# Performance work log

Hardware: AMD Instinct MI355X
Metric: run time of the kernel (lower is better)

## Reference

```python
import jax, jax.numpy as jnp
import numpy as np

N, E, R = 50000, 800000, 3
D, H = 128, 128
NUM_SHAPE, NUM_COLOR, MAX_POS = 16, 8, 25
B, NUM_CLASS = 256, 10
EPS = 1e-5


def setup_inputs() -> dict:
    key = jax.random.key(0)
    ks = jax.random.split(key, 24)
    s = lambda fan: 1.0 / np.sqrt(fan)
    inp = {
        "x_idx": jax.random.randint(ks[0], (N, 3), 0, 8),
        "edge_index": jax.random.randint(ks[1], (2, E), 0, N),
        "edge_type": jax.random.randint(ks[2], (E,), 0, R),
        "batch": jnp.sort(jax.random.randint(ks[3], (N,), 0, B)),
        "shape_emb": jax.random.normal(ks[4], (NUM_SHAPE, D), jnp.float32),
        "color_emb": jax.random.normal(ks[5], (NUM_COLOR, D), jnp.float32),
        "pos_emb": jax.random.normal(ks[6], (MAX_POS, D), jnp.float32),
        "W1": jax.random.normal(ks[7], (R, D, H), jnp.float32) * s(D),
        "root1": jax.random.normal(ks[8], (D, H), jnp.float32) * s(D),
        "b1": jax.random.normal(ks[9], (H,), jnp.float32) * 0.01,
        "g1": jax.random.uniform(ks[10], (H,), jnp.float32, 0.5, 1.5),
        "beta1": jax.random.normal(ks[11], (H,), jnp.float32) * 0.1,
        "m1": jax.random.normal(ks[12], (H,), jnp.float32) * 0.1,
        "v1": jax.random.uniform(ks[13], (H,), jnp.float32, 0.5, 1.5),
        "W2": jax.random.normal(ks[14], (R, H, H), jnp.float32) * s(H),
        "root2": jax.random.normal(ks[15], (H, H), jnp.float32) * s(H),
        "b2": jax.random.normal(ks[16], (H,), jnp.float32) * 0.01,
        "g2": jax.random.uniform(ks[17], (H,), jnp.float32, 0.5, 1.5),
        "beta2": jax.random.normal(ks[18], (H,), jnp.float32) * 0.1,
        "m2": jax.random.normal(ks[19], (H,), jnp.float32) * 0.1,
        "v2": jax.random.uniform(ks[20], (H,), jnp.float32, 0.5, 1.5),
        "clsW": jax.random.normal(ks[21], (H, NUM_CLASS), jnp.float32) * s(H),
        "clsb": jax.random.normal(ks[22], (NUM_CLASS,), jnp.float32) * 0.01,
    }
    return inp


def rgcn_conv(x, edge_index, edge_type, W, root, b):
    # per-relation transform, gather at src, mean-scatter at dst (PyG RGCNConv, aggr='mean')
    src, dst = edge_index[0], edge_index[1]
    xw = jnp.einsum('nd,rdh->rnh', x, W)            # [R, N, H]
    msg = xw[edge_type, src]                        # [E, H]
    seg = dst * R + edge_type                       # segment per (dst, relation)
    ssum = jax.ops.segment_sum(msg, seg, num_segments=N * R)
    cnt = jax.ops.segment_sum(jnp.ones((E,), x.dtype), seg, num_segments=N * R)
    mean = jnp.where(cnt[:, None] > 0, ssum / jnp.maximum(cnt, 1.0)[:, None], 0.0)
    agg = mean.reshape(N, R, -1).sum(axis=1)        # sum over relations of per-relation means
    return agg + x @ root + b


def batchnorm_eval(x, g, beta, m, v):
    return g * (x - m) * jax.lax.rsqrt(v + EPS) + beta


def reference(x_idx, edge_index, edge_type, batch, shape_emb, color_emb, pos_emb,
              W1, root1, b1, g1, beta1, m1, v1,
              W2, root2, b2, g2, beta2, m2, v2, clsW, clsb):
    x = (shape_emb[x_idx[:, 0]] + color_emb[x_idx[:, 1]]
         + pos_emb[jnp.clip(x_idx[:, 2], 0, MAX_POS - 1)])
    x = jax.nn.relu(batchnorm_eval(rgcn_conv(x, edge_index, edge_type, W1, root1, b1),
                                   g1, beta1, m1, v1))
    x = jax.nn.relu(batchnorm_eval(rgcn_conv(x, edge_index, edge_type, W2, root2, b2),
                                   g2, beta2, m2, v2))
    hsum = jax.ops.segment_sum(x, batch, num_segments=B)
    hcnt = jax.ops.segment_sum(jnp.ones((N,), x.dtype), batch, num_segments=B)
    hg = hsum / jnp.maximum(hcnt, 1.0)[:, None]     # global mean pool [B, H]
    return hg @ clsW + clsb
```

## Files before the change

kernel.cpp:

```cpp
#include <hip/hip_runtime.h>

#define N_NODES 50000
#define E_EDGES 800000
#define R_REL 3
#define NSEG (N_NODES * R_REL)
#define DH 128
#define KDIM 512
#define ROWB 1024
#define XOFF (3 * DH * 2)
#define BATCHES 256
#define NCLASS 10
#define EPSV 1e-5f

#define BSHIFT 9
#define BNODES 512
#define NBUCK ((N_NODES + BNODES - 1) / BNODES)
#define SEGB (BNODES * R_REL)
#define CAP 9216
#define NCHUNK 128
#define CHUNK (E_EDGES / NCHUNK)
#define MATN (NBUCK * NCHUNK)

typedef __attribute__((ext_vector_type(8))) short short8v;
typedef __attribute__((ext_vector_type(4))) unsigned uint4v;
typedef __attribute__((ext_vector_type(4))) float float4v;
typedef unsigned short ushort_t;

__device__ __forceinline__ ushort_t f2bf(float f) {
    union { float f; unsigned u; } x; x.f = f;
    unsigned r = x.u + 0x7FFFu + ((x.u >> 16) & 1u);
    return (ushort_t)(r >> 16);
}
__device__ __forceinline__ float bf2f(ushort_t h) {
    union { unsigned u; float f; } x; x.u = ((unsigned)h) << 16;
    return x.f;
}
__device__ __forceinline__ float u2f(unsigned u) {
    union { unsigned u; float f; } x; x.u = u;
    return x.f;
}

__global__ void build_x_kernel(const int* __restrict__ xi,
                               const float* __restrict__ se,
                               const float* __restrict__ ce,
                               const float* __restrict__ pe,
                               ushort_t* __restrict__ A) {
    int tid = blockIdx.x * blockDim.x + threadIdx.x;
    int node = tid >> 4, c = tid & 15;
    if (node >= N_NODES) return;
    int i0 = xi[node * 3 + 0];
    int i1 = xi[node * 3 + 1];
    int i2 = xi[node * 3 + 2];
    i2 = i2 < 0 ? 0 : (i2 > 24 ? 24 : i2);
    const float4* sa = reinterpret_cast<const float4*>(se + (size_t)i0 * DH + c * 8);
    const float4* sb = reinterpret_cast<const float4*>(ce + (size_t)i1 * DH + c * 8);
    const float4* sp = reinterpret_cast<const float4*>(pe + (size_t)i2 * DH + c * 8);
    short8v o;
    #pragma unroll
    for (int q = 0; q < 2; ++q) {
        float4 a = sa[q], b = sb[q], p = sp[q];
        o[q * 4 + 0] = (short)f2bf(a.x + b.x + p.x);
        o[q * 4 + 1] = (short)f2bf(a.y + b.y + p.y);
        o[q * 4 + 2] = (short)f2bf(a.z + b.z + p.z);
        o[q * 4 + 3] = (short)f2bf(a.w + b.w + p.w);
    }
    *reinterpret_cast<short8v*>(A + (size_t)node * KDIM + 3 * DH + c * 8) = o;
}

__global__ __launch_bounds__(512) void chunk_hist_kernel(const int* __restrict__ ei,
                                                         int* __restrict__ mat) {
    __shared__ int lh[NBUCK];
    int t = threadIdx.x, blk = blockIdx.x;
    if (t < NBUCK) lh[t] = 0;
    __syncthreads();
    int base = blk * CHUNK;
    for (int i = t; i < CHUNK; i += 512)
        atomicAdd(&lh[ei[E_EDGES + base + i] >> BSHIFT], 1);
    __syncthreads();
    if (t < NBUCK) mat[t * NCHUNK + blk] = lh[t];
}

__global__ __launch_bounds__(1024) void matscan_kernel(int* __restrict__ mat,
                                                       int* __restrict__ bbase,
                                                       int* __restrict__ offs3) {
    __shared__ int partial[1024];
    int t = threadIdx.x;
    int buf[13];
    int base = t * 13;
    int s = 0;
    #pragma unroll
    for (int j = 0; j < 13; ++j) {
        int idx = base + j;
        int v = (idx < MATN) ? mat[idx] : 0;
        buf[j] = s;
        s += v;
    }
    partial[t] = s;
    __syncthreads();
    for (int d = 1; d < 1024; d <<= 1) {
        int u = (t >= d) ? partial[t - d] : 0;
        __syncthreads();
        partial[t] += u;
        __syncthreads();
    }
    int off = (t > 0) ? partial[t - 1] : 0;
    #pragma unroll
    for (int j = 0; j < 13; ++j) {
        int idx = base + j;
        if (idx < MATN) mat[idx] = off + buf[j];
    }
    __syncthreads();
    if (t < NBUCK) bbase[t] = mat[t * NCHUNK];
    if (t == 0) { bbase[NBUCK] = E_EDGES; offs3[NSEG] = E_EDGES; }
}

__global__ __launch_bounds__(512) void chunk_scatter_kernel(const int* __restrict__ ei,
                                                            const int* __restrict__ et,
                                                            const int* __restrict__ mat,
                                                            int* __restrict__ tlist) {
    __shared__ int sorted[CHUNK];
    __shared__ int lh[NBUCK];
    __shared__ int lstart[NBUCK + 1];
    __shared__ int mbase[NBUCK];
    __shared__ int scr[128];
    int t = threadIdx.x, blk = blockIdx.x;
    if (t < NBUCK) { lh[t] = 0; mbase[t] = mat[t * NCHUNK + blk]; }
    __syncthreads();
    int base = blk * CHUNK;
    for (int i = t; i < CHUNK; i += 512)
        atomicAdd(&lh[ei[E_EDGES + base + i] >> BSHIFT], 1);
    __syncthreads();
    if (t < 128) scr[t] = (t < NBUCK) ? lh[t] : 0;
    __syncthreads();
    for (int d = 1; d < 128; d <<= 1) {
        int u = 0;
        if (t < 128 && t >= d) u = scr[t - d];
        __syncthreads();
        if (t < 128) scr[t] += u;
        __syncthreads();
    }
    if (t < NBUCK) lstart[t] = scr[t] - lh[t];
    if (t == NBUCK - 1) lstart[NBUCK] = scr[t];
    __syncthreads();
    if (t < NBUCK) lh[t] = lstart[t];
    __syncthreads();
    for (int i = t; i < CHUNK; i += 512) {
        int e = base + i;
        int src = ei[e];
        int dst = ei[E_EDGES + e];
        int r = et[e];
        int b = dst >> BSHIFT;
        int ls = (dst & (BNODES - 1)) * R_REL + r;
        int p = atomicAdd(&lh[b], 1);
        sorted[p] = (ls << 16) | src;
    }
    __syncthreads();
    for (int i = t; i < CHUNK; i += 512) {
        int lo = 0, hi = NBUCK - 1;
        while (lo < hi) {
            int mid = (lo + hi + 1) >> 1;
            if (lstart[mid] <= i) lo = mid; else hi = mid - 1;
        }
        tlist[mbase[lo] + (i - lstart[lo])] = sorted[i];
    }
}

__global__ __launch_bounds__(512) void localsort_kernel(const int* __restrict__ tlist,
                                                        const int* __restrict__ bbase,
                                                        int* __restrict__ offs3,
                                                        int* __restrict__ elist) {
    __shared__ int hist[SEGB];
    __shared__ int scr[512];
    __shared__ int tl[CAP];
    __shared__ int el[CAP];
    int b = blockIdx.x, t = threadIdx.x;
    int ebeg = bbase[b], eend = bbase[b + 1];
    int cnt = eend - ebeg;
    int segbase = b * SEGB;
    #pragma unroll
    for (int j = 0; j < 3; ++j) hist[t + j * 512] = 0;
    __syncthreads();

    bool fit = (cnt <= CAP);
    if (fit) {
        for (int i = t; i < cnt; i += 512) {
            int pk = tlist[ebeg + i];
            tl[i] = pk;
            atomicAdd(&hist[pk >> 16], 1);
        }
    } else {
        for (int i = t; i < cnt; i += 512)
            atomicAdd(&hist[tlist[ebeg + i] >> 16], 1);
    }
    __syncthreads();
    int h0 = hist[3 * t], h1 = hist[3 * t + 1], h2 = hist[3 * t + 2];
    int s = h0 + h1 + h2;
    scr[t] = s;
    __syncthreads();
    for (int d = 1; d < 512; d <<= 1) {
        int u = (t >= d) ? scr[t - d] : 0;
        __syncthreads();
        scr[t] += u;
        __syncthreads();
    }
    int off = (t > 0) ? scr[t - 1] : 0;
    int e0 = off, e1 = off + h0, e2 = off + h0 + h1;
    {
        int sg = segbase + 3 * t;
        if (sg < NSEG)     offs3[sg]     = ebeg + e0;
        if (sg + 1 < NSEG) offs3[sg + 1] = ebeg + e1;
        if (sg + 2 < NSEG) offs3[sg + 2] = ebeg + e2;
    }
    __syncthreads();
    hist[3 * t] = e0; hist[3 * t + 1] = e1; hist[3 * t + 2] = e2;
    __syncthreads();
    if (fit) {
        for (int i = t; i < cnt; i += 512) {
            int pk = tl[i];
            int pos = atomicAdd(&hist[pk >> 16], 1);
            el[pos] = (pk & 0xFFFF) * ROWB + XOFF;
        }
        __syncthreads();
        for (int i = t; i < cnt; i += 512)
            elist[ebeg + i] = el[i];
    } else {
        for (int i = t; i < cnt; i += 512) {
            int pk = tlist[ebeg + i];
            int pos = atomicAdd(&hist[pk >> 16], 1);
            elist[ebeg + pos] = (pk & 0xFFFF) * ROWB + XOFF;
        }
    }
}

__global__ void setup_kernel(const float* __restrict__ W1, const float* __restrict__ root1,
                             const float* __restrict__ W2, const float* __restrict__ root2,
                             ushort_t* __restrict__ Wf1, ushort_t* __restrict__ Wf2,
                             const int* __restrict__ batch, int* __restrict__ bstart,
                             const float* __restrict__ b1, const float* __restrict__ g1,
                             const float* __restrict__ be1, const float* __restrict__ m1,
                             const float* __restrict__ v1,
                             const float* __restrict__ b2, const float* __restrict__ g2,
                             const float* __restrict__ be2, const float* __restrict__ m2,
                             const float* __restrict__ v2,
                             float* __restrict__ sc1, float* __restrict__ sh1,
                             float* __restrict__ sc2, float* __restrict__ sh2) {
    int tid = blockIdx.x * blockDim.x + threadIdx.x;
    if (tid < 16384) {
        int L = tid >> 13;
        int rem = tid & 8191;
        int l = rem & 63;
        int nt = (rem >> 6) & 7;
        int ks = rem >> 9;
        const float* W = L ? W2 : W1;
        const float* root = L ? root2 : root1;
        ushort_t* dst = (L ? Wf2 : Wf1) + (size_t)rem * 8;
        int col = nt * 16 + (l & 15);
        int kb = ks * 32 + (l >> 4) * 8;
        short8v o;
        #pragma unroll
        for (int j = 0; j < 8; ++j) {
            int k = kb + j;
            float w = (k < 384) ? W[(size_t)k * DH + col] : root[(size_t)(k - 384) * DH + col];
            o[j] = (short)f2bf(w);
        }
        *reinterpret_cast<short8v*>(dst) = o;
    } else if (tid < 16384 + BATCHES + 1) {
        int b = tid - 16384;
        int lo = 0, hi = N_NODES;
        while (lo < hi) {
            int mid = (lo + hi) >> 1;
            if (batch[mid] < b) lo = mid + 1; else hi = mid;
        }
        bstart[b] = lo;
    } else if (tid < 16384 + 257 + DH) {
        int c = tid - 16384 - 257;
        float s = g1[c] * rsqrtf(v1[c] + EPSV);
        sc1[c] = s;
        sh1[c] = (b1[c] - m1[c]) * s + be1[c];
    } else if (tid < 16384 + 257 + 2 * DH) {
        int c = tid - 16384 - 257 - DH;
        float s = g2[c] * rsqrtf(v2[c] + EPSV);
        sc2[c] = s;
        sh2[c] = (b2[c] - m2[c]) * s + be2[c];
    }
}

__global__ __launch_bounds__(256) void agg_kernel(const char* __restrict__ Ab,
                                                  const int* __restrict__ offs3,
                                                  const int* __restrict__ elist,
                                                  char* __restrict__ Aob) {
    int t = threadIdx.x;
    int g = t >> 4, c = t & 15;
    int n = blockIdx.x * 16 + g;
    if (n >= N_NODES) return;
    int s0 = offs3[3 * n + 0];
    int s1 = offs3[3 * n + 1];
    int s2 = offs3[3 * n + 2];
    int s3 = offs3[3 * n + 3];
    int cb = c * 16;

    float S0 = 0, S1 = 0, S2 = 0, S3 = 0, S4 = 0, S5 = 0, S6 = 0, S7 = 0;
    float p0 = 0, p1 = 0, p2 = 0, p3 = 0, p4 = 0, p5 = 0, p6 = 0, p7 = 0;
    float q0 = 0, q1 = 0, q2 = 0, q3 = 0, q4 = 0, q5 = 0, q6 = 0, q7 = 0;

    #define ACC8(V)                                           \
        S0 += u2f(V[0] << 16); S1 += u2f(V[0] & 0xFFFF0000u); \
        S2 += u2f(V[1] << 16); S3 += u2f(V[1] & 0xFFFF0000u); \
        S4 += u2f(V[2] << 16); S5 += u2f(V[2] & 0xFFFF0000u); \
        S6 += u2f(V[3] << 16); S7 += u2f(V[3] & 0xFFFF0000u);
    #define SNAPCHK(E)                                                              \
        if ((E) == s1) { p0=S0; p1=S1; p2=S2; p3=S3; p4=S4; p5=S5; p6=S6; p7=S7; }  \
        if ((E) == s2) { q0=S0; q1=S1; q2=S2; q3=S3; q4=S4; q5=S5; q6=S6; q7=S7; }

    int i = s0;
    int bend = s0 + ((s3 - s0) & ~3);
    if (i < bend) {
        int j0 = elist[i], j1 = elist[i + 1], j2 = elist[i + 2], j3 = elist[i + 3];
        uint4v g0 = *reinterpret_cast<const uint4v*>(Ab + j0 + cb);
        uint4v g1 = *reinterpret_cast<const uint4v*>(Ab + j1 + cb);
        uint4v g2 = *reinterpret_cast<const uint4v*>(Ab + j2 + cb);
        uint4v g3 = *reinterpret_cast<const uint4v*>(Ab + j3 + cb);
        for (;;) {
            int inx = i + 4;
            bool more = inx < bend;
            uint4v h0, h1, h2, h3;
            if (more) {
                int k0 = elist[inx], k1 = elist[inx + 1], k2 = elist[inx + 2], k3 = elist[inx + 3];
                h0 = *reinterpret_cast<const uint4v*>(Ab + k0 + cb);
                h1 = *reinterpret_cast<const uint4v*>(Ab + k1 + cb);
                h2 = *reinterpret_cast<const uint4v*>(Ab + k2 + cb);
                h3 = *reinterpret_cast<const uint4v*>(Ab + k3 + cb);
            }
            SNAPCHK(i)     ACC8(g0)
            SNAPCHK(i + 1) ACC8(g1)
            SNAPCHK(i + 2) ACC8(g2)
            SNAPCHK(i + 3) ACC8(g3)
            if (!more) break;
            g0 = h0; g1 = h1; g2 = h2; g3 = h3;
            i = inx;
        }
        i = bend;
    }
    for (; i < s3; ++i) {
        int j = elist[i];
        uint4v v = *reinterpret_cast<const uint4v*>(Ab + j + cb);
        SNAPCHK(i)
        ACC8(v)
    }
    if (s1 == s3) { p0=S0; p1=S1; p2=S2; p3=S3; p4=S4; p5=S5; p6=S6; p7=S7; }
    if (s2 == s3) { q0=S0; q1=S1; q2=S2; q3=S3; q4=S4; q5=S5; q6=S6; q7=S7; }
    #undef ACC8
    #undef SNAPCHK

    int c0 = s1 - s0, c1 = s2 - s1, c2 = s3 - s2;
    float i0 = c0 ? 1.f / c0 : 0.f;
    float i1 = c1 ? 1.f / c1 : 0.f;
    float i2 = c2 ? 1.f / c2 : 0.f;
    char* base = Aob + (size_t)n * ROWB + cb;
    uint4v o;
    o[0] = (unsigned)f2bf(p0 * i0) | ((unsigned)f2bf(p1 * i0) << 16);
    o[1] = (unsigned)f2bf(p2 * i0) | ((unsigned)f2bf(p3 * i0) << 16);
    o[2] = (unsigned)f2bf(p4 * i0) | ((unsigned)f2bf(p5 * i0) << 16);
    o[3] = (unsigned)f2bf(p6 * i0) | ((unsigned)f2bf(p7 * i0) << 16);
    *reinterpret_cast<uint4v*>(base + 0 * 256) = o;
    o[0] = (unsigned)f2bf((q0 - p0) * i1) | ((unsigned)f2bf((q1 - p1) * i1) << 16);
    o[1] = (unsigned)f2bf((q2 - p2) * i1) | ((unsigned)f2bf((q3 - p3) * i1) << 16);
    o[2] = (unsigned)f2bf((q4 - p4) * i1) | ((unsigned)f2bf((q5 - p5) * i1) << 16);
    o[3] = (unsigned)f2bf((q6 - p6) * i1) | ((unsigned)f2bf((q7 - p7) * i1) << 16);
    *reinterpret_cast<uint4v*>(base + 1 * 256) = o;
    o[0] = (unsigned)f2bf((S0 - q0) * i2) | ((unsigned)f2bf((S1 - q1) * i2) << 16);
    o[1] = (unsigned)f2bf((S2 - q2) * i2) | ((unsigned)f2bf((S3 - q3) * i2) << 16);
    o[2] = (unsigned)f2bf((S4 - q4) * i2) | ((unsigned)f2bf((S5 - q5) * i2) << 16);
    o[3] = (unsigned)f2bf((S6 - q6) * i2) | ((unsigned)f2bf((S7 - q7) * i2) << 16);
    *reinterpret_cast<uint4v*>(base + 2 * 256) = o;
}

__global__ __launch_bounds__(256) void gemm_mfma_kernel(const ushort_t* __restrict__ A,
                                                        const ushort_t* __restrict__ Wf,
                                                        const float* __restrict__ sc,
                                                        const float* __restrict__ sh,
                                                        ushort_t* __restrict__ Aout) {
    int w = threadIdx.x >> 6, l = threadIdx.x & 63;
    int base = blockIdx.x * 64 + w * 16;
    int arow = base + (l & 15);
    if (arow >= N_NODES) arow = N_NODES - 1;
    const short8v* ap = reinterpret_cast<const short8v*>(A + (size_t)arow * KDIM + (l >> 4) * 8);
    const short8v* wf = reinterpret_cast<const short8v*>(Wf) + l;

    float4v acc[8];
    #pragma unroll
    for (int nt = 0; nt < 8; ++nt) acc[nt] = (float4v){0.f, 0.f, 0.f, 0.f};

    #pragma unroll 4
    for (int ks = 0; ks < 16; ++ks) {
        short8v a = ap[ks * 4];
        const short8v* bp = wf + ks * 512;
        #pragma unroll
        for (int nt = 0; nt < 8; ++nt) {
            short8v b = bp[nt * 64];
            acc[nt] = __builtin_amdgcn_mfma_f32_16x16x32_bf16(a, b, acc[nt], 0, 0, 0);
        }
    }

    int colb = l & 15;
    int rowq = (l >> 4) * 4;
    #pragma unroll
    for (int nt = 0; nt < 8; ++nt) {
        int col = nt * 16 + colb;
        float scv = sc[col], shv = sh[col];
        #pragma unroll
        for (int r = 0; r < 4; ++r) {
            int row = base + rowq + r;
            if (row < N_NODES) {
                float val = fmaxf(acc[nt][r] * scv + shv, 0.f);
                Aout[(size_t)row * KDIM + 3 * DH + col] = f2bf(val);
            }
        }
    }
}

__global__ __launch_bounds__(256) void pool_cls_kernel(
        const ushort_t* __restrict__ h,
        const int* __restrict__ bstart,
        const float* __restrict__ clsW,
        const float* __restrict__ clsb,
        float* __restrict__ out) {
    __shared__ float hsh[DH];
    int b = blockIdx.x;
    int t = threadIdx.x;
    int c = t & 127;
    int half = t >> 7;
    int beg = bstart[b], end = bstart[b + 1];
    float s = 0.f;
    for (int n = beg + half; n < end; n += 2)
        s += bf2f(h[(size_t)n * KDIM + c]);
    if (half == 1) hsh[c] = s;
    __syncthreads();
    if (half == 0) {
        float cnt = (float)(end - beg);
        float inv = cnt > 0.f ? 1.f / cnt : 1.f;
        hsh[c] = (s + hsh[c]) * inv;
    }
    __syncthreads();
    if (t < NCLASS) {
        float acc = clsb[t];
        #pragma unroll 16
        for (int d = 0; d < DH; ++d)
            acc += hsh[d] * clsW[d * NCLASS + t];
        out[b * NCLASS + t] = acc;
    }
}

extern "C" void kernel_launch(void* const* d_in, const int* in_sizes, int n_in,
                              void* d_out, int out_size, void* d_ws, size_t ws_size,
                              hipStream_t stream) {
    const int*   x_idx  = (const int*)d_in[0];
    const int*   eidx   = (const int*)d_in[1];
    const int*   etype  = (const int*)d_in[2];
    const int*   batch  = (const int*)d_in[3];
    const float* se     = (const float*)d_in[4];
    const float* ce     = (const float*)d_in[5];
    const float* pe     = (const float*)d_in[6];
    const float* W1     = (const float*)d_in[7];
    const float* root1  = (const float*)d_in[8];
    const float* b1     = (const float*)d_in[9];
    const float* g1     = (const float*)d_in[10];
    const float* beta1  = (const float*)d_in[11];
    const float* m1     = (const float*)d_in[12];
    const float* v1     = (const float*)d_in[13];
    const float* W2     = (const float*)d_in[14];
    const float* root2  = (const float*)d_in[15];
    const float* b2     = (const float*)d_in[16];
    const float* g2     = (const float*)d_in[17];
    const float* beta2  = (const float*)d_in[18];
    const float* m2     = (const float*)d_in[19];
    const float* v2     = (const float*)d_in[20];
    const float* clsW   = (const float*)d_in[21];
    const float* clsb   = (const float*)d_in[22];
    float* out = (float*)d_out;

    char* ws = (char*)d_ws;
    const size_t A_bytes     = (size_t)N_NODES * KDIM * 2;
    const size_t elist_bytes = (size_t)E_EDGES * 4;
    const size_t tlist_bytes = (size_t)E_EDGES * 4;
    const size_t offs3_pad   = 600064;
    ushort_t* A      = (ushort_t*)(ws);
    int*      elist  = (int*)(ws + A_bytes);
    int*      tlist  = (int*)(ws + A_bytes + elist_bytes);
    int*      offs3  = (int*)(ws + A_bytes + elist_bytes + tlist_bytes);
    char*     p      = ws + A_bytes + elist_bytes + tlist_bytes + offs3_pad;
    int*      mat    = (int*)p;            p += 50176;
    int*      bbase  = (int*)p;            p += 512;
    int*      bstart = (int*)p;            p += 1088;
    ushort_t* Wf1    = (ushort_t*)p;       p += 131072;
    ushort_t* Wf2    = (ushort_t*)p;       p += 131072;
    float*    sc1    = (float*)p;          p += 512;
    float*    sh1    = (float*)p;          p += 512;
    float*    sc2    = (float*)p;          p += 512;
    float*    sh2    = (float*)p;          p += 512;

    const int TB = 256;

    build_x_kernel<<<(N_NODES * 16 + TB - 1) / TB, TB, 0, stream>>>(x_idx, se, ce, pe, A);

    setup_kernel<<<67, 256, 0, stream>>>(W1, root1, W2, root2, Wf1, Wf2,
                                         batch, bstart,
                                         b1, g1, beta1, m1, v1,
                                         b2, g2, beta2, m2, v2,
                                         sc1, sh1, sc2, sh2);

    chunk_hist_kernel<<<NCHUNK, 512, 0, stream>>>(eidx, mat);
    matscan_kernel<<<1, 1024, 0, stream>>>(mat, bbase, offs3);
    chunk_scatter_kernel<<<NCHUNK, 512, 0, stream>>>(eidx, etype, mat, tlist);
    localsort_kernel<<<NBUCK, 512, 0, stream>>>(tlist, bbase, offs3, elist);

    agg_kernel<<<(N_NODES + 15) / 16, 256, 0, stream>>>((const char*)A, offs3, elist, (char*)A);
    gemm_mfma_kernel<<<(N_NODES + 63) / 64, 256, 0, stream>>>(A, Wf1, sc1, sh1, A);

    agg_kernel<<<(N_NODES + 15) / 16, 256, 0, stream>>>((const char*)A, offs3, elist, (char*)A);
    gemm_mfma_kernel<<<(N_NODES + 63) / 64, 256, 0, stream>>>(A, Wf2, sc2, sh2, A);

    pool_cls_kernel<<<BATCHES, 256, 0, stream>>>(A + 3 * DH, bstart, clsW, clsb, out);
}
```

Before: 222.1 us.

## Slice feature rows into column chunks, fuse preprocessing kernels, widen GEMM tiles

Lays out each node row as four 256-byte slices, each holding three relation-mean chunks and one feature chunk, and launches aggregation with a second grid dimension over slices. Each thread now gathers 4 bytes per edge instead of 16, so a slice's gather working set is smaller and may stay in cache better. The embedding build, edge histogram and setup kernels are merged into one launch to cut launch overhead. The GEMM now computes 32 rows per wave, and layer 2 writes to a separate compact buffer that the pooling kernel reads. The trade-off is four times as many gather iterations and edge-list reads in the aggregation kernel.

After: 289.7 us. 1.3x slower.

```diff
diff --git a/kernel.cpp b/kernel.cpp
--- a/kernel.cpp
+++ b/kernel.cpp
@@ -7,7 +7,6 @@
 #define DH 128
 #define KDIM 512
 #define ROWB 1024
-#define XOFF (3 * DH * 2)
 #define BATCHES 256
 #define NCLASS 10
 #define EPSV 1e-5f
@@ -21,8 +20,11 @@
 #define CHUNK (E_EDGES / NCHUNK)
 #define MATN (NBUCK * NCHUNK)
 
+#define PRE_BX 3125
+#define PRE_H (PRE_BX + NCHUNK)
+#define PRE_S (PRE_H + 67)
+
 typedef __attribute__((ext_vector_type(8))) short short8v;
-typedef __attribute__((ext_vector_type(4))) unsigned uint4v;
 typedef __attribute__((ext_vector_type(4))) float float4v;
 typedef unsigned short ushort_t;
 
@@ -39,45 +41,104 @@
     union { unsigned u; float f; } x; x.u = u;
     return x.f;
 }
-
-__global__ void build_x_kernel(const int* __restrict__ xi,
-                               const float* __restrict__ se,
-                               const float* __restrict__ ce,
-                               const float* __restrict__ pe,
-                               ushort_t* __restrict__ A) {
-    int tid = blockIdx.x * blockDim.x + threadIdx.x;
-    int node = tid >> 4, c = tid & 15;
-    if (node >= N_NODES) return;
-    int i0 = xi[node * 3 + 0];
-    int i1 = xi[node * 3 + 1];
-    int i2 = xi[node * 3 + 2];
-    i2 = i2 < 0 ? 0 : (i2 > 24 ? 24 : i2);
-    const float4* sa = reinterpret_cast<const float4*>(se + (size_t)i0 * DH + c * 8);
-    const float4* sb = reinterpret_cast<const float4*>(ce + (size_t)i1 * DH + c * 8);
-    const float4* sp = reinterpret_cast<const float4*>(pe + (size_t)i2 * DH + c * 8);
-    short8v o;
-    #pragma unroll
-    for (int q = 0; q < 2; ++q) {
-        float4 a = sa[q], b = sb[q], p = sp[q];
-        o[q * 4 + 0] = (short)f2bf(a.x + b.x + p.x);
-        o[q * 4 + 1] = (short)f2bf(a.y + b.y + p.y);
-        o[q * 4 + 2] = (short)f2bf(a.z + b.z + p.z);
-        o[q * 4 + 3] = (short)f2bf(a.w + b.w + p.w);
-    }
-    *reinterpret_cast<short8v*>(A + (size_t)node * KDIM + 3 * DH + c * 8) = o;
-}
-
-__global__ __launch_bounds__(512) void chunk_hist_kernel(const int* __restrict__ ei,
-                                                         int* __restrict__ mat) {
+__device__ __forceinline__ unsigned pack2(float lo, float hi) {
+    return (unsigned)f2bf(lo) | ((unsigned)f2bf(hi) << 16);
+}
+
+__global__ __launch_bounds__(256) void pre_kernel(
+        const int* __restrict__ xi, const float* __restrict__ se,
+        const float* __restrict__ ce, const float* __restrict__ pe,
+        ushort_t* __restrict__ A,
+        const int* __restrict__ ei, int* __restrict__ mat,
+        const float* __restrict__ W1, const float* __restrict__ root1,
+        const float* __restrict__ W2, const float* __restrict__ root2,
+        ushort_t* __restrict__ Wf1, ushort_t* __restrict__ Wf2,
+        const int* __restrict__ batch, int* __restrict__ bstart,
+        const float* __restrict__ b1, const float* __restrict__ g1,
+        const float* __restrict__ be1, const float* __restrict__ m1,
+        const float* __restrict__ v1,
+        const float* __restrict__ b2, const float* __restrict__ g2,
+        const float* __restrict__ be2, const float* __restrict__ m2,
+        const float* __restrict__ v2,
+        float* __restrict__ sc1, float* __restrict__ sh1,
+        float* __restrict__ sc2, float* __restrict__ sh2) {
     __shared__ int lh[NBUCK];
-    int t = threadIdx.x, blk = blockIdx.x;
-    if (t < NBUCK) lh[t] = 0;
-    __syncthreads();
-    int base = blk * CHUNK;
-    for (int i = t; i < CHUNK; i += 512)
-        atomicAdd(&lh[ei[E_EDGES + base + i] >> BSHIFT], 1);
-    __syncthreads();
-    if (t < NBUCK) mat[t * NCHUNK + blk] = lh[t];
+    int blk = blockIdx.x, t = threadIdx.x;
+    if (blk < PRE_BX) {
+        int tid = blk * 256 + t;
+        int node = tid >> 4, c = tid & 15;
+        int i0 = xi[node * 3 + 0];
+        int i1 = xi[node * 3 + 1];
+        int i2 = xi[node * 3 + 2];
+        i2 = i2 < 0 ? 0 : (i2 > 24 ? 24 : i2);
+        const float4* sa = reinterpret_cast<const float4*>(se + (size_t)i0 * DH + c * 8);
+        const float4* sb = reinterpret_cast<const float4*>(ce + (size_t)i1 * DH + c * 8);
+        const float4* sp = reinterpret_cast<const float4*>(pe + (size_t)i2 * DH + c * 8);
+        short8v o;
+        #pragma unroll
+        for (int q = 0; q < 2; ++q) {
+            float4 a = sa[q], b = sb[q], p = sp[q];
+            o[q * 4 + 0] = (short)f2bf(a.x + b.x + p.x);
+            o[q * 4 + 1] = (short)f2bf(a.y + b.y + p.y);
+            o[q * 4 + 2] = (short)f2bf(a.z + b.z + p.z);
+            o[q * 4 + 3] = (short)f2bf(a.w + b.w + p.w);
+        }
+        int elem = (c >> 2) * 128 + 96 + (c & 3) * 8;
+        *reinterpret_cast<short8v*>(A + (size_t)node * KDIM + elem) = o;
+    } else if (blk < PRE_H) {
+        int ch = blk - PRE_BX;
+        if (t < NBUCK) lh[t] = 0;
+        __syncthreads();
+        int base = ch * CHUNK;
+        for (int i = t; i < CHUNK; i += 256)
+            atomicAdd(&lh[ei[E_EDGES + base + i] >> BSHIFT], 1);
+        __syncthreads();
+        if (t < NBUCK) mat[t * NCHUNK + ch] = lh[t];
+    } else if (blk < PRE_S) {
+        int tid = (blk - PRE_H) * 256 + t;
+        if (tid < 16384) {
+            int L = tid >> 13;
+            int rem = tid & 8191;
+            int l = rem & 63;
+            int nt = (rem >> 6) & 7;
+            int ks = rem >> 9;
+            const float* W = L ? W2 : W1;
+            const float* root = L ? root2 : root1;
+            ushort_t* dst = (L ? Wf2 : Wf1) + (size_t)rem * 8;
+            int col = nt * 16 + (l & 15);
+            int kb = ks * 32 + (l >> 4) * 8;
+            short8v o;
+            #pragma unroll
+            for (int j = 0; j < 8; ++j) {
+                int kp = kb + j;
+                int s = kp >> 7, rm = kp & 127;
+                int pcs = rm >> 5, f = rm & 31;
+                int k = pcs * 128 + s * 32 + f;
+                float w = (k < 384) ? W[(size_t)k * DH + col]
+                                    : root[(size_t)(k - 384) * DH + col];
+                o[j] = (short)f2bf(w);
+            }
+            *reinterpret_cast<short8v*>(dst) = o;
+        } else if (tid < 16384 + BATCHES + 1) {
+            int b = tid - 16384;
+            int lo = 0, hi = N_NODES;
+            while (lo < hi) {
+                int mid = (lo + hi) >> 1;
+                if (batch[mid] < b) lo = mid + 1; else hi = mid;
+            }
+            bstart[b] = lo;
+        } else if (tid < 16384 + 257 + DH) {
+            int c = tid - 16384 - 257;
+            float s = g1[c] * rsqrtf(v1[c] + EPSV);
+            sc1[c] = s;
+            sh1[c] = (b1[c] - m1[c]) * s + be1[c];
+        } else if (tid < 16384 + 257 + 2 * DH) {
+            int c = tid - 16384 - 257 - DH;
+            float s = g2[c] * rsqrtf(v2[c] + EPSV);
+            sc2[c] = s;
+            sh2[c] = (b2[c] - m2[c]) * s + be2[c];
+        }
+    }
 }
 
 __global__ __launch_bounds__(1024) void matscan_kernel(int* __restrict__ mat,
@@ -218,7 +279,7 @@
         for (int i = t; i < cnt; i += 512) {
             int pk = tl[i];
             int pos = atomicAdd(&hist[pk >> 16], 1);
-            el[pos] = (pk & 0xFFFF) * ROWB + XOFF;
+            el[pos] = (pk & 0xFFFF) * ROWB + 192;
         }
         __syncthreads();
         for (int i = t; i < cnt; i += 512)
@@ -227,61 +288,8 @@
         for (int i = t; i < cnt; i += 512) {
             int pk = tlist[ebeg + i];
             int pos = atomicAdd(&hist[pk >> 16], 1);
-            elist[ebeg + pos] = (pk & 0xFFFF) * ROWB + XOFF;
-        }
-    }
-}
-
-__global__ void setup_kernel(const float* __restrict__ W1, const float* __restrict__ root1,
-                             const float* __restrict__ W2, const float* __restrict__ root2,
-                             ushort_t* __restrict__ Wf1, ushort_t* __restrict__ Wf2,
-                             const int* __restrict__ batch, int* __restrict__ bstart,
-                             const float* __restrict__ b1, const float* __restrict__ g1,
-                             const float* __restrict__ be1, const float* __restrict__ m1,
-                             const float* __restrict__ v1,
-                             const float* __restrict__ b2, const float* __restrict__ g2,
-                             const float* __restrict__ be2, const float* __restrict__ m2,
-                             const float* __restrict__ v2,
-                             float* __restrict__ sc1, float* __restrict__ sh1,
-                             float* __restrict__ sc2, float* __restrict__ sh2) {
-    int tid = blockIdx.x * blockDim.x + threadIdx.x;
-    if (tid < 16384) {
-        int L = tid >> 13;
-        int rem = tid & 8191;
-        int l = rem & 63;
-        int nt = (rem >> 6) & 7;
-        int ks = rem >> 9;
-        const float* W = L ? W2 : W1;
-        const float* root = L ? root2 : root1;
-        ushort_t* dst = (L ? Wf2 : Wf1) + (size_t)rem * 8;
-        int col = nt * 16 + (l & 15);
-        int kb = ks * 32 + (l >> 4) * 8;
-        short8v o;
-        #pragma unroll
-        for (int j = 0; j < 8; ++j) {
-            int k = kb + j;
-            float w = (k < 384) ? W[(size_t)k * DH + col] : root[(size_t)(k - 384) * DH + col];
-            o[j] = (short)f2bf(w);
-        }
-        *reinterpret_cast<short8v*>(dst) = o;
-    } else if (tid < 16384 + BATCHES + 1) {
-        int b = tid - 16384;
-        int lo = 0, hi = N_NODES;
-        while (lo < hi) {
-            int mid = (lo + hi) >> 1;
-            if (batch[mid] < b) lo = mid + 1; else hi = mid;
-        }
-        bstart[b] = lo;
-    } else if (tid < 16384 + 257 + DH) {
-        int c = tid - 16384 - 257;
-        float s = g1[c] * rsqrtf(v1[c] + EPSV);
-        sc1[c] = s;
-        sh1[c] = (b1[c] - m1[c]) * s + be1[c];
-    } else if (tid < 16384 + 257 + 2 * DH) {
-        int c = tid - 16384 - 257 - DH;
-        float s = g2[c] * rsqrtf(v2[c] + EPSV);
-        sc2[c] = s;
-        sh2[c] = (b2[c] - m2[c]) * s + be2[c];
+            elist[ebeg + pos] = (pk & 0xFFFF) * ROWB + 192;
+        }
     }
 }
 
@@ -292,49 +300,43 @@
     int t = threadIdx.x;
     int g = t >> 4, c = t & 15;
     int n = blockIdx.x * 16 + g;
-    if (n >= N_NODES) return;
+    int sb = blockIdx.y * 256;
     int s0 = offs3[3 * n + 0];
     int s1 = offs3[3 * n + 1];
     int s2 = offs3[3 * n + 2];
     int s3 = offs3[3 * n + 3];
-    int cb = c * 16;
-
-    float S0 = 0, S1 = 0, S2 = 0, S3 = 0, S4 = 0, S5 = 0, S6 = 0, S7 = 0;
-    float p0 = 0, p1 = 0, p2 = 0, p3 = 0, p4 = 0, p5 = 0, p6 = 0, p7 = 0;
-    float q0 = 0, q1 = 0, q2 = 0, q3 = 0, q4 = 0, q5 = 0, q6 = 0, q7 = 0;
-
-    #define ACC8(V)                                           \
-        S0 += u2f(V[0] << 16); S1 += u2f(V[0] & 0xFFFF0000u); \
-        S2 += u2f(V[1] << 16); S3 += u2f(V[1] & 0xFFFF0000u); \
-        S4 += u2f(V[2] << 16); S5 += u2f(V[2] & 0xFFFF0000u); \
-        S6 += u2f(V[3] << 16); S7 += u2f(V[3] & 0xFFFF0000u);
-    #define SNAPCHK(E)                                                              \
-        if ((E) == s1) { p0=S0; p1=S1; p2=S2; p3=S3; p4=S4; p5=S5; p6=S6; p7=S7; }  \
-        if ((E) == s2) { q0=S0; q1=S1; q2=S2; q3=S3; q4=S4; q5=S5; q6=S6; q7=S7; }
+    const char* gb = Ab + sb + c * 4;
+
+    float Sl = 0, Sh = 0, pl = 0, ph = 0, ql = 0, qh = 0;
+
+    #define ACC(V) { Sl += u2f((V) << 16); Sh += u2f((V) & 0xFFFF0000u); }
+    #define SNAP(E) { if ((E) == s1) { pl = Sl; ph = Sh; } \
+                      if ((E) == s2) { ql = Sl; qh = Sh; } }
 
     int i = s0;
     int bend = s0 + ((s3 - s0) & ~3);
     if (i < bend) {
         int j0 = elist[i], j1 = elist[i + 1], j2 = elist[i + 2], j3 = elist[i + 3];
-        uint4v g0 = *reinterpret_cast<const uint4v*>(Ab + j0 + cb);
-        uint4v g1 = *reinterpret_cast<const uint4v*>(Ab + j1 + cb);
-        uint4v g2 = *reinterpret_cast<const uint4v*>(Ab + j2 + cb);
-        uint4v g3 = *reinterpret_cast<const uint4v*>(Ab + j3 + cb);
+        unsigned g0 = *reinterpret_cast<const unsigned*>(gb + j0);
+        unsigned g1 = *reinterpret_cast<const unsigned*>(gb + j1);
+        unsigned g2 = *reinterpret_cast<const unsigned*>(gb + j2);
+        unsigned g3 = *reinterpret_cast<const unsigned*>(gb + j3);
         for (;;) {
             int inx = i + 4;
             bool more = inx < bend;
-            uint4v h0, h1, h2, h3;
+            unsigned h0 = 0, h1 = 0, h2 = 0, h3 = 0;
             if (more) {
-                int k0 = elist[inx], k1 = elist[inx + 1], k2 = elist[inx + 2], k3 = elist[inx + 3];
-                h0 = *reinterpret_cast<const uint4v*>(Ab + k0 + cb);
-                h1 = *reinterpret_cast<const uint4v*>(Ab + k1 + cb);
-                h2 = *reinterpret_cast<const uint4v*>(Ab + k2 + cb);
-                h3 = *reinterpret_cast<const uint4v*>(Ab + k3 + cb);
+                int k0 = elist[inx], k1 = elist[inx + 1];
+                int k2 = elist[inx + 2], k3 = elist[inx + 3];
+                h0 = *reinterpret_cast<const unsigned*>(gb + k0);
+                h1 = *reinterpret_cast<const unsigned*>(gb + k1);
+                h2 = *reinterpret_cast<const unsigned*>(gb + k2);
+                h3 = *reinterpret_cast<const unsigned*>(gb + k3);
             }
-            SNAPCHK(i)     ACC8(g0)
-            SNAPCHK(i + 1) ACC8(g1)
-            SNAPCHK(i + 2) ACC8(g2)
-            SNAPCHK(i + 3) ACC8(g3)
+            SNAP(i)     ACC(g0)
+            SNAP(i + 1) ACC(g1)
+            SNAP(i + 2) ACC(g2)
+            SNAP(i + 3) ACC(g3)
             if (!more) break;
             g0 = h0; g1 = h1; g2 = h2; g3 = h3;
             i = inx;
@@ -342,78 +344,80 @@
         i = bend;
     }
     for (; i < s3; ++i) {
-        int j = elist[i];
-        uint4v v = *reinterpret_cast<const uint4v*>(Ab + j + cb);
-        SNAPCHK(i)
-        ACC8(v)
-    }
-    if (s1 == s3) { p0=S0; p1=S1; p2=S2; p3=S3; p4=S4; p5=S5; p6=S6; p7=S7; }
-    if (s2 == s3) { q0=S0; q1=S1; q2=S2; q3=S3; q4=S4; q5=S5; q6=S6; q7=S7; }
-    #undef ACC8
-    #undef SNAPCHK
+        unsigned v = *reinterpret_cast<const unsigned*>(gb + elist[i]);
+        SNAP(i)
+        ACC(v)
+    }
+    if (s1 == s3) { pl = Sl; ph = Sh; }
+    if (s2 == s3) { ql = Sl; qh = Sh; }
+    #undef ACC
+    #undef SNAP
 
     int c0 = s1 - s0, c1 = s2 - s1, c2 = s3 - s2;
     float i0 = c0 ? 1.f / c0 : 0.f;
     float i1 = c1 ? 1.f / c1 : 0.f;
     float i2 = c2 ? 1.f / c2 : 0.f;
-    char* base = Aob + (size_t)n * ROWB + cb;
-    uint4v o;
-    o[0] = (unsigned)f2bf(p0 * i0) | ((unsigned)f2bf(p1 * i0) << 16);
-    o[1] = (unsigned)f2bf(p2 * i0) | ((unsigned)f2bf(p3 * i0) << 16);
-    o[2] = (unsigned)f2bf(p4 * i0) | ((unsigned)f2bf(p5 * i0) << 16);
-    o[3] = (unsigned)f2bf(p6 * i0) | ((unsigned)f2bf(p7 * i0) << 16);
-    *reinterpret_cast<uint4v*>(base + 0 * 256) = o;
-    o[0] = (unsigned)f2bf((q0 - p0) * i1) | ((unsigned)f2bf((q1 - p1) * i1) << 16);
-    o[1] = (unsigned)f2bf((q2 - p2) * i1) | ((unsigned)f2bf((q3 - p3) * i1) << 16);
-    o[2] = (unsigned)f2bf((q4 - p4) * i1) | ((unsigned)f2bf((q5 - p5) * i1) << 16);
-    o[3] = (unsigned)f2bf((q6 - p6) * i1) | ((unsigned)f2bf((q7 - p7) * i1) << 16);
-    *reinterpret_cast<uint4v*>(base + 1 * 256) = o;
-    o[0] = (unsigned)f2bf((S0 - q0) * i2) | ((unsigned)f2bf((S1 - q1) * i2) << 16);
-    o[1] = (unsigned)f2bf((S2 - q2) * i2) | ((unsigned)f2bf((S3 - q3) * i2) << 16);
-    o[2] = (unsigned)f2bf((S4 - q4) * i2) | ((unsigned)f2bf((S5 - q5) * i2) << 16);
-    o[3] = (unsigned)f2bf((S6 - q6) * i2) | ((unsigned)f2bf((S7 - q7) * i2) << 16);
-    *reinterpret_cast<uint4v*>(base + 2 * 256) = o;
+    char* base = Aob + (size_t)n * ROWB + sb + c * 4;
+    *reinterpret_cast<unsigned*>(base + 0)   = pack2(pl * i0, ph * i0);
+    *reinterpret_cast<unsigned*>(base + 64)  = pack2((ql - pl) * i1, (qh - ph) * i1);
+    *reinterpret_cast<unsigned*>(base + 128) = pack2((Sl - ql) * i2, (Sh - qh) * i2);
 }
 
 __global__ __launch_bounds__(256) void gemm_mfma_kernel(const ushort_t* __restrict__ A,
                                                         const ushort_t* __restrict__ Wf,
                                                         const float* __restrict__ sc,
                                                         const float* __restrict__ sh,
-                                                        ushort_t* __restrict__ Aout) {
+                                                        ushort_t* __restrict__ Aout,
+                                                        int sliced) {
     int w = threadIdx.x >> 6, l = threadIdx.x & 63;
-    int base = blockIdx.x * 64 + w * 16;
-    int arow = base + (l & 15);
-    if (arow >= N_NODES) arow = N_NODES - 1;
-    const short8v* ap = reinterpret_cast<const short8v*>(A + (size_t)arow * KDIM + (l >> 4) * 8);
+    int base = blockIdx.x * 128 + w * 32;
+    int ra = base + (l & 15);
+    int rb = ra + 16;
+    int rac = ra >= N_NODES ? N_NODES - 1 : ra;
+    int rbc = rb >= N_NODES ? N_NODES - 1 : rb;
+    const short8v* apa = reinterpret_cast<const short8v*>(A + (size_t)rac * KDIM + (l >> 4) * 8);
+    const short8v* apb = reinterpret_cast<const short8v*>(A + (size_t)rbc * KDIM + (l >> 4) * 8);
     const short8v* wf = reinterpret_cast<const short8v*>(Wf) + l;
 
-    float4v acc[8];
+    float4v acc0[8], acc1[8];
     #pragma unroll
-    for (int nt = 0; nt < 8; ++nt) acc[nt] = (float4v){0.f, 0.f, 0.f, 0.f};
+    for (int nt = 0; nt < 8; ++nt) {
+        acc0[nt] = (float4v){0.f, 0.f, 0.f, 0.f};
+        acc1[nt] = (float4v){0.f, 0.f, 0.f, 0.f};
+    }
 
     #pragma unroll 4
     for (int ks = 0; ks < 16; ++ks) {
-        short8v a = ap[ks * 4];
+        short8v a0 = apa[ks * 4];
+        short8v a1 = apb[ks * 4];
         const short8v* bp = wf + ks * 512;
         #pragma unroll
         for (int nt = 0; nt < 8; ++nt) {
             short8v b = bp[nt * 64];
-            acc[nt] = __builtin_amdgcn_mfma_f32_16x16x32_bf16(a, b, acc[nt], 0, 0, 0);
+            acc0[nt] = __builtin_amdgcn_mfma_f32_16x16x32_bf16(a0, b, acc0[nt], 0, 0, 0);
+            acc1[nt] = __builtin_amdgcn_mfma_f32_16x16x32_bf16(a1, b, acc1[nt], 0, 0, 0);
         }
     }
 
     int colb = l & 15;
     int rowq = (l >> 4) * 4;
+    int ostride = sliced ? KDIM : DH;
     #pragma unroll
     for (int nt = 0; nt < 8; ++nt) {
         int col = nt * 16 + colb;
+        int off = sliced ? ((col >> 5) * 128 + 96 + (col & 31)) : col;
         float scv = sc[col], shv = sh[col];
         #pragma unroll
         for (int r = 0; r < 4; ++r) {
-            int row = base + rowq + r;
-            if (row < N_NODES) {
-                float val = fmaxf(acc[nt][r] * scv + shv, 0.f);
-                Aout[(size_t)row * KDIM + 3 * DH + col] = f2bf(val);
+            int row0 = base + rowq + r;
+            int row1 = row0 + 16;
+            if (row0 < N_NODES) {
+                float v0 = fmaxf(acc0[nt][r] * scv + shv, 0.f);
+                Aout[(size_t)row0 * ostride + off] = f2bf(v0);
+            }
+            if (row1 < N_NODES) {
+                float v1 = fmaxf(acc1[nt][r] * scv + shv, 0.f);
+                Aout[(size_t)row1 * ostride + off] = f2bf(v1);
             }
         }
     }
@@ -433,7 +437,7 @@
     int beg = bstart[b], end = bstart[b + 1];
     float s = 0.f;
     for (int n = beg + half; n < end; n += 2)
-        s += bf2f(h[(size_t)n * KDIM + c]);
+        s += bf2f(h[(size_t)n * DH + c]);
     if (half == 1) hsh[c] = s;
     __syncthreads();
     if (half == 0) {
@@ -498,27 +502,25 @@
     float*    sh1    = (float*)p;          p += 512;
     float*    sc2    = (float*)p;          p += 512;
     float*    sh2    = (float*)p;          p += 512;
-
-    const int TB = 256;
-
-    build_x_kernel<<<(N_NODES * 16 + TB - 1) / TB, TB, 0, stream>>>(x_idx, se, ce, pe, A);
-
-    setup_kernel<<<67, 256, 0, stream>>>(W1, root1, W2, root2, Wf1, Wf2,
-                                         batch, bstart,
-                                         b1, g1, beta1, m1, v1,
-                                         b2, g2, beta2, m2, v2,
-                                         sc1, sh1, sc2, sh2);
-
-    chunk_hist_kernel<<<NCHUNK, 512, 0, stream>>>(eidx, mat);
+    ushort_t* H2     = (ushort_t*)p;       p += (size_t)N_NODES * DH * 2;
+
+    pre_kernel<<<PRE_S, 256, 0, stream>>>(x_idx, se, ce, pe, A,
+                                          eidx, mat,
+                                          W1, root1, W2, root2, Wf1, Wf2,
+                                          batch, bstart,
+                                          b1, g1, beta1, m1, v1,
+                                          b2, g2, beta2, m2, v2,
+                                          sc1, sh1, sc2, sh2);
+
     matscan_kernel<<<1, 1024, 0, stream>>>(mat, bbase, offs3);
     chunk_scatter_kernel<<<NCHUNK, 512, 0, stream>>>(eidx, etype, mat, tlist);
     localsort_kernel<<<NBUCK, 512, 0, stream>>>(tlist, bbase, offs3, elist);
 
-    agg_kernel<<<(N_NODES + 15) / 16, 256, 0, stream>>>((const char*)A, offs3, elist, (char*)A);
-    gemm_mfma_kernel<<<(N_NODES + 63) / 64, 256, 0, stream>>>(A, Wf1, sc1, sh1, A);
-
-    agg_kernel<<<(N_NODES + 15) / 16, 256, 0, stream>>>((const char*)A, offs3, elist, (char*)A);
-    gemm_mfma_kernel<<<(N_NODES + 63) / 64, 256, 0, stream>>>(A, Wf2, sc2, sh2, A);
-
-    pool_cls_kernel<<<BATCHES, 256, 0, stream>>>(A + 3 * DH, bstart, clsW, clsb, out);
-}
+    agg_kernel<<<dim3(N_NODES / 16, 4), 256, 0, stream>>>((const char*)A, offs3, elist, (char*)A);
+    gemm_mfma_kernel<<<(N_NODES + 127) / 128, 256, 0, stream>>>(A, Wf1, sc1, sh1, A, 1);
+
+    agg_kernel<<<dim3(N_NODES / 16, 4), 256, 0, stream>>>((const char*)A, offs3, elist, (char*)A);
+    gemm_mfma_kernel<<<(N_NODES + 127) / 128, 256, 0, stream>>>(A, Wf2, sc2, sh2, H2, 0);
+
+    pool_cls_kernel<<<BATCHES, 256, 0, stream>>>(H2, bstart, clsW, clsb, out);
+}
```

## Merge setup kernels into one launch, double GEMM rows per wave, compact layer-2 output

Applied to the files above, without the earlier changes.

Folds the embedding build, edge histogram and weight/BN/batch setup into a single pre_kernel dispatched by block range, cutting two launches. The MFMA GEMM now gives each wave 32 rows, reusing every loaded weight fragment for two A tiles, and launches half as many blocks. The second layer writes to a compact N×128 buffer, so the pooling kernel reads contiguous rows. It also drops the bounds check in agg_kernel, which is safe only because N is divisible by 16, and it doubles the accumulator registers.

New measurement: 251.2 us. +13.1%, slower.

```diff
diff --git a/kernel.cpp b/kernel.cpp
--- a/kernel.cpp
+++ b/kernel.cpp
@@ -21,6 +21,10 @@
 #define CHUNK (E_EDGES / NCHUNK)
 #define MATN (NBUCK * NCHUNK)
 
+#define PRE_BX 3125
+#define PRE_H (PRE_BX + NCHUNK)
+#define PRE_S (PRE_H + 67)
+
 typedef __attribute__((ext_vector_type(8))) short short8v;
 typedef __attribute__((ext_vector_type(4))) unsigned uint4v;
 typedef __attribute__((ext_vector_type(4))) float float4v;
@@ -40,44 +44,96 @@
     return x.f;
 }
 
-__global__ void build_x_kernel(const int* __restrict__ xi,
-                               const float* __restrict__ se,
-                               const float* __restrict__ ce,
-                               const float* __restrict__ pe,
-                               ushort_t* __restrict__ A) {
-    int tid = blockIdx.x * blockDim.x + threadIdx.x;
-    int node = tid >> 4, c = tid & 15;
-    if (node >= N_NODES) return;
-    int i0 = xi[node * 3 + 0];
-    int i1 = xi[node * 3 + 1];
-    int i2 = xi[node * 3 + 2];
-    i2 = i2 < 0 ? 0 : (i2 > 24 ? 24 : i2);
-    const float4* sa = reinterpret_cast<const float4*>(se + (size_t)i0 * DH + c * 8);
-    const float4* sb = reinterpret_cast<const float4*>(ce + (size_t)i1 * DH + c * 8);
-    const float4* sp = reinterpret_cast<const float4*>(pe + (size_t)i2 * DH + c * 8);
-    short8v o;
-    #pragma unroll
-    for (int q = 0; q < 2; ++q) {
-        float4 a = sa[q], b = sb[q], p = sp[q];
-        o[q * 4 + 0] = (short)f2bf(a.x + b.x + p.x);
-        o[q * 4 + 1] = (short)f2bf(a.y + b.y + p.y);
-        o[q * 4 + 2] = (short)f2bf(a.z + b.z + p.z);
-        o[q * 4 + 3] = (short)f2bf(a.w + b.w + p.w);
-    }
-    *reinterpret_cast<short8v*>(A + (size_t)node * KDIM + 3 * DH + c * 8) = o;
-}
-
-__global__ __launch_bounds__(512) void chunk_hist_kernel(const int* __restrict__ ei,
-                                                         int* __restrict__ mat) {
+__global__ __launch_bounds__(256) void pre_kernel(
+        const int* __restrict__ xi, const float* __restrict__ se,
+        const float* __restrict__ ce, const float* __restrict__ pe,
+        ushort_t* __restrict__ A,
+        const int* __restrict__ ei, int* __restrict__ mat,
+        const float* __restrict__ W1, const float* __restrict__ root1,
+        const float* __restrict__ W2, const float* __restrict__ root2,
+        ushort_t* __restrict__ Wf1, ushort_t* __restrict__ Wf2,
+        const int* __restrict__ batch, int* __restrict__ bstart,
+        const float* __restrict__ b1, const float* __restrict__ g1,
+        const float* __restrict__ be1, const float* __restrict__ m1,
+        const float* __restrict__ v1,
+        const float* __restrict__ b2, const float* __restrict__ g2,
+        const float* __restrict__ be2, const float* __restrict__ m2,
+        const float* __restrict__ v2,
+        float* __restrict__ sc1, float* __restrict__ sh1,
+        float* __restrict__ sc2, float* __restrict__ sh2) {
     __shared__ int lh[NBUCK];
-    int t = threadIdx.x, blk = blockIdx.x;
-    if (t < NBUCK) lh[t] = 0;
-    __syncthreads();
-    int base = blk * CHUNK;
-    for (int i = t; i < CHUNK; i += 512)
-        atomicAdd(&lh[ei[E_EDGES + base + i] >> BSHIFT], 1);
-    __syncthreads();
-    if (t < NBUCK) mat[t * NCHUNK + blk] = lh[t];
+    int blk = blockIdx.x, t = threadIdx.x;
+    if (blk < PRE_BX) {
+        int tid = blk * 256 + t;
+        int node = tid >> 4, c = tid & 15;
+        int i0 = xi[node * 3 + 0];
+        int i1 = xi[node * 3 + 1];
+        int i2 = xi[node * 3 + 2];
+        i2 = i2 < 0 ? 0 : (i2 > 24 ? 24 : i2);
+        const float4* sa = reinterpret_cast<const float4*>(se + (size_t)i0 * DH + c * 8);
+        const float4* sb = reinterpret_cast<const float4*>(ce + (size_t)i1 * DH + c * 8);
+        const float4* sp = reinterpret_cast<const float4*>(pe + (size_t)i2 * DH + c * 8);
+        short8v o;
+        #pragma unroll
+        for (int q = 0; q < 2; ++q) {
+            float4 a = sa[q], b = sb[q], p = sp[q];
+            o[q * 4 + 0] = (short)f2bf(a.x + b.x + p.x);
+            o[q * 4 + 1] = (short)f2bf(a.y + b.y + p.y);
+            o[q * 4 + 2] = (short)f2bf(a.z + b.z + p.z);
+            o[q * 4 + 3] = (short)f2bf(a.w + b.w + p.w);
+        }
+        *reinterpret_cast<short8v*>(A + (size_t)node * KDIM + 3 * DH + c * 8) = o;
+    } else if (blk < PRE_H) {
+        int ch = blk - PRE_BX;
+        if (t < NBUCK) lh[t] = 0;
+        __syncthreads();
+        int base = ch * CHUNK;
+        for (int i = t; i < CHUNK; i += 256)
+            atomicAdd(&lh[ei[E_EDGES + base + i] >> BSHIFT], 1);
+        __syncthreads();
+        if (t < NBUCK) mat[t * NCHUNK + ch] = lh[t];
+    } else if (blk < PRE_S) {
+        int tid = (blk - PRE_H) * 256 + t;
+        if (tid < 16384) {
+            int L = tid >> 13;
+            int rem = tid & 8191;
+            int l = rem & 63;
+            int nt = (rem >> 6) & 7;
+            int ks = rem >> 9;
+            const float* W = L ? W2 : W1;
+            const float* root = L ? root2 : root1;
+            ushort_t* dst = (L ? Wf2 : Wf1) + (size_t)rem * 8;
+            int col = nt * 16 + (l & 15);
+            int kb = ks * 32 + (l >> 4) * 8;
+            short8v o;
+            #pragma unroll
+            for (int j = 0; j < 8; ++j) {
+                int k = kb + j;
+                float w = (k < 384) ? W[(size_t)k * DH + col]
+                                    : root[(size_t)(k - 384) * DH + col];
+                o[j] = (short)f2bf(w);
+            }
+            *reinterpret_cast<short8v*>(dst) = o;
+        } else if (tid < 16384 + BATCHES + 1) {
+            int b = tid - 16384;
+            int lo = 0, hi = N_NODES;
+            while (lo < hi) {
+                int mid = (lo + hi) >> 1;
+                if (batch[mid] < b) lo = mid + 1; else hi = mid;
+            }
+            bstart[b] = lo;
+        } else if (tid < 16384 + 257 + DH) {
+            int c = tid - 16384 - 257;
+            float s = g1[c] * rsqrtf(v1[c] + EPSV);
+            sc1[c] = s;
+            sh1[c] = (b1[c] - m1[c]) * s + be1[c];
+        } else if (tid < 16384 + 257 + 2 * DH) {
+            int c = tid - 16384 - 257 - DH;
+            float s = g2[c] * rsqrtf(v2[c] + EPSV);
+            sc2[c] = s;
+            sh2[c] = (b2[c] - m2[c]) * s + be2[c];
+        }
+    }
 }
 
 __global__ __launch_bounds__(1024) void matscan_kernel(int* __restrict__ mat,
@@ -232,59 +288,6 @@
     }
 }
 
-__global__ void setup_kernel(const float* __restrict__ W1, const float* __restrict__ root1,
-                             const float* __restrict__ W2, const float* __restrict__ root2,
-                             ushort_t* __restrict__ Wf1, ushort_t* __restrict__ Wf2,
-                             const int* __restrict__ batch, int* __restrict__ bstart,
-                             const float* __restrict__ b1, const float* __restrict__ g1,
-                             const float* __restrict__ be1, const float* __restrict__ m1,
-                             const float* __restrict__ v1,
-                             const float* __restrict__ b2, const float* __restrict__ g2,
-                             const float* __restrict__ be2, const float* __restrict__ m2,
-                             const float* __restrict__ v2,
-                             float* __restrict__ sc1, float* __restrict__ sh1,
-                             float* __restrict__ sc2, float* __restrict__ sh2) {
-    int tid = blockIdx.x * blockDim.x + threadIdx.x;
-    if (tid < 16384) {
-        int L = tid >> 13;
-        int rem = tid & 8191;
-        int l = rem & 63;
-        int nt = (rem >> 6) & 7;
-        int ks = rem >> 9;
-        const float* W = L ? W2 : W1;
-        const float* root = L ? root2 : root1;
-        ushort_t* dst = (L ? Wf2 : Wf1) + (size_t)rem * 8;
-        int col = nt * 16 + (l & 15);
-        int kb = ks * 32 + (l >> 4) * 8;
-        short8v o;
-        #pragma unroll
-        for (int j = 0; j < 8; ++j) {
-            int k = kb + j;
-            float w = (k < 384) ? W[(size_t)k * DH + col] : root[(size_t)(k - 384) * DH + col];
-            o[j] = (short)f2bf(w);
-        }
-        *reinterpret_cast<short8v*>(dst) = o;
-    } else if (tid < 16384 + BATCHES + 1) {
-        int b = tid - 16384;
-        int lo = 0, hi = N_NODES;
-        while (lo < hi) {
-            int mid = (lo + hi) >> 1;
-            if (batch[mid] < b) lo = mid + 1; else hi = mid;
-        }
-        bstart[b] = lo;
-    } else if (tid < 16384 + 257 + DH) {
-        int c = tid - 16384 - 257;
-        float s = g1[c] * rsqrtf(v1[c] + EPSV);
-        sc1[c] = s;
-        sh1[c] = (b1[c] - m1[c]) * s + be1[c];
-    } else if (tid < 16384 + 257 + 2 * DH) {
-        int c = tid - 16384 - 257 - DH;
-        float s = g2[c] * rsqrtf(v2[c] + EPSV);
-        sc2[c] = s;
-        sh2[c] = (b2[c] - m2[c]) * s + be2[c];
-    }
-}
-
 __global__ __launch_bounds__(256) void agg_kernel(const char* __restrict__ Ab,
                                                   const int* __restrict__ offs3,
                                                   const int* __restrict__ elist,
@@ -292,7 +295,6 @@
     int t = threadIdx.x;
     int g = t >> 4, c = t & 15;
     int n = blockIdx.x * 16 + g;
-    if (n >= N_NODES) return;
     int s0 = offs3[3 * n + 0];
     int s1 = offs3[3 * n + 1];
     int s2 = offs3[3 * n + 2];
@@ -379,26 +381,35 @@
                                                         const ushort_t* __restrict__ Wf,
                                                         const float* __restrict__ sc,
                                                         const float* __restrict__ sh,
-                                                        ushort_t* __restrict__ Aout) {
+                                                        ushort_t* __restrict__ Aout,
+                                                        int ostride, int ooff) {
     int w = threadIdx.x >> 6, l = threadIdx.x & 63;
-    int base = blockIdx.x * 64 + w * 16;
-    int arow = base + (l & 15);
-    if (arow >= N_NODES) arow = N_NODES - 1;
-    const short8v* ap = reinterpret_cast<const short8v*>(A + (size_t)arow * KDIM + (l >> 4) * 8);
+    int base = blockIdx.x * 128 + w * 32;
+    int ra = base + (l & 15);
+    int rb = ra + 16;
+    int rac = ra >= N_NODES ? N_NODES - 1 : ra;
+    int rbc = rb >= N_NODES ? N_NODES - 1 : rb;
+    const short8v* apa = reinterpret_cast<const short8v*>(A + (size_t)rac * KDIM + (l >> 4) * 8);
+    const short8v* apb = reinterpret_cast<const short8v*>(A + (size_t)rbc * KDIM + (l >> 4) * 8);
     const short8v* wf = reinterpret_cast<const short8v*>(Wf) + l;
 
-    float4v acc[8];
+    float4v acc0[8], acc1[8];
     #pragma unroll
-    for (int nt = 0; nt < 8; ++nt) acc[nt] = (float4v){0.f, 0.f, 0.f, 0.f};
+    for (int nt = 0; nt < 8; ++nt) {
+        acc0[nt] = (float4v){0.f, 0.f, 0.f, 0.f};
+        acc1[nt] = (float4v){0.f, 0.f, 0.f, 0.f};
+    }
 
     #pragma unroll 4
     for (int ks = 0; ks < 16; ++ks) {
-        short8v a = ap[ks * 4];
+        short8v a0 = apa[ks * 4];
+        short8v a1 = apb[ks * 4];
         const short8v* bp = wf + ks * 512;
         #pragma unroll
         for (int nt = 0; nt < 8; ++nt) {
             short8v b = bp[nt * 64];
-            acc[nt] = __builtin_amdgcn_mfma_f32_16x16x32_bf16(a, b, acc[nt], 0, 0, 0);
+            acc0[nt] = __builtin_amdgcn_mfma_f32_16x16x32_bf16(a0, b, acc0[nt], 0, 0, 0);
+            acc1[nt] = __builtin_amdgcn_mfma_f32_16x16x32_bf16(a1, b, acc1[nt], 0, 0, 0);
         }
     }
 
@@ -410,10 +421,15 @@
         float scv = sc[col], shv = sh[col];
         #pragma unroll
         for (int r = 0; r < 4; ++r) {
-            int row = base + rowq + r;
-            if (row < N_NODES) {
-                float val = fmaxf(acc[nt][r] * scv + shv, 0.f);
-                Aout[(size_t)row * KDIM + 3 * DH + col] = f2bf(val);
+            int row0 = base + rowq + r;
+            int row1 = row0 + 16;
+            if (row0 < N_NODES) {
+                float v0 = fmaxf(acc0[nt][r] * scv + shv, 0.f);
+                Aout[(size_t)row0 * ostride + ooff + col] = f2bf(v0);
+            }
+            if (row1 < N_NODES) {
+                float v1 = fmaxf(acc1[nt][r] * scv + shv, 0.f);
+                Aout[(size_t)row1 * ostride + ooff + col] = f2bf(v1);
             }
         }
     }
@@ -433,7 +449,7 @@
     int beg = bstart[b], end = bstart[b + 1];
     float s = 0.f;
     for (int n = beg + half; n < end; n += 2)
-        s += bf2f(h[(size_t)n * KDIM + c]);
+        s += bf2f(h[(size_t)n * DH + c]);
     if (half == 1) hsh[c] = s;
     __syncthreads();
     if (half == 0) {
@@ -498,27 +514,27 @@
     float*    sh1    = (float*)p;          p += 512;
     float*    sc2    = (float*)p;          p += 512;
     float*    sh2    = (float*)p;          p += 512;
-
-    const int TB = 256;
-
-    build_x_kernel<<<(N_NODES * 16 + TB - 1) / TB, TB, 0, stream>>>(x_idx, se, ce, pe, A);
-
-    setup_kernel<<<67, 256, 0, stream>>>(W1, root1, W2, root2, Wf1, Wf2,
-                                         batch, bstart,
-                                         b1, g1, beta1, m1, v1,
-                                         b2, g2, beta2, m2, v2,
-                                         sc1, sh1, sc2, sh2);
-
-    chunk_hist_kernel<<<NCHUNK, 512, 0, stream>>>(eidx, mat);
+    ushort_t* H2     = (ushort_t*)p;       p += (size_t)N_NODES * DH * 2;
+
+    pre_kernel<<<PRE_S, 256, 0, stream>>>(x_idx, se, ce, pe, A,
+                                          eidx, mat,
+                                          W1, root1, W2, root2, Wf1, Wf2,
+                                          batch, bstart,
+                                          b1, g1, beta1, m1, v1,
+                                          b2, g2, beta2, m2, v2,
+                                          sc1, sh1, sc2, sh2);
+
     matscan_kernel<<<1, 1024, 0, stream>>>(mat, bbase, offs3);
     chunk_scatter_kernel<<<NCHUNK, 512, 0, stream>>>(eidx, etype, mat, tlist);
     localsort_kernel<<<NBUCK, 512, 0, stream>>>(tlist, bbase, offs3, elist);
 
-    agg_kernel<<<(N_NODES + 15) / 16, 256, 0, stream>>>((const char*)A, offs3, elist, (char*)A);
-    gemm_mfma_kernel<<<(N_NODES + 63) / 64, 256, 0, stream>>>(A, Wf1, sc1, sh1, A);
-
-    agg_kernel<<<(N_NODES + 15) / 16, 256, 0, stream>>>((const char*)A, offs3, elist, (char*)A);
-    gemm_mfma_kernel<<<(N_NODES + 63) / 64, 256, 0, stream>>>(A, Wf2, sc2, sh2, A);
-
-    pool_cls_kernel<<<BATCHES, 256, 0, stream>>>(A + 3 * DH, bstart, clsW, clsb, out);
-}
+    agg_kernel<<<N_NODES / 16, 256, 0, stream>>>((const char*)A, offs3, elist, (char*)A);
+    gemm_mfma_kernel<<<(N_NODES + 127) / 128, 256, 0, stream>>>(A, Wf1, sc1, sh1,
+                                                                A, KDIM, 3 * DH);
+
+    agg_kernel<<<N_NODES / 16, 256, 0, stream>>>((const char*)A, offs3, elist, (char*)A);
+    gemm_mfma_kernel<<<(N_NODES + 127) / 128, 256, 0, stream>>>(A, Wf2, sc2, sh2,
+                                                                H2, DH, 0);
+
+    pool_cls_kernel<<<BATCHES, 256, 0, stream>>>(H2, bstart, clsW, clsb, out);
+}
```
